# Kernel optimization log

Hardware: AMD Instinct MI355X
Metric: run time of the kernel (lower is better)

## Reference

```python
import jax, jax.numpy as jnp
import numpy as np

B_, L_, D_, N_ = 4, 4096, 64, 16
DT = 0.1
EPS = 1e-6


def _complex_log(x):
    # log|x| (clamped) + i*pi for negative entries, matching torch impl
    real = jnp.log(jnp.maximum(jnp.abs(x), EPS))
    imag = jnp.where(x < 0, jnp.float32(np.pi), jnp.float32(0.0))
    return jax.lax.complex(real, imag)


def _clogaddexp(a, b):
    # stable complex log(exp(a)+exp(b)) using max of real parts
    m = jnp.maximum(a.real, b.real)
    return jnp.log(jnp.exp(a - m) + jnp.exp(b - m)) + m


def _clogcumsumexp(x, axis):
    return jax.lax.associative_scan(_clogaddexp, x, axis=axis)


def setup_inputs() -> dict:
    key = jax.random.key(0)
    ks = jax.random.split(key, 6)
    x = jax.random.normal(ks[0], (B_, L_, D_), jnp.float32)
    s = 1.0 / np.sqrt(D_)
    Wb = jax.random.uniform(ks[1], (N_, D_), jnp.float32, -s, s)
    bb = jax.random.uniform(ks[2], (N_,), jnp.float32, -s, s)
    Wc = jax.random.uniform(ks[3], (N_, D_), jnp.float32, -s, s)
    bc = jax.random.uniform(ks[4], (N_,), jnp.float32, -s, s)
    Wd = jax.random.uniform(ks[5], (1, D_), jnp.float32, -s, s)
    bd = jnp.zeros((1,), jnp.float32)
    # S4D-Real init: A_n = -(n+1), repeated over input_dim rows -> (D, N)
    A = jnp.tile(-(jnp.arange(N_, dtype=jnp.float32) + 1.0)[None, :], (D_, 1))
    return {"x": x, "A": A, "Wb": Wb, "bb": bb, "Wc": Wc, "bc": bc,
            "Wd": Wd, "bd": bd}


def reference(x, A, Wb, bb, Wc, bc, Wd, bd):
    # projections: (b,l,n)
    Bm = x @ Wb.T + bb
    Cm = x @ Wc.T + bc
    # delta network: softplus(linear(x)) + dt, broadcast to input_dim
    delta = jax.nn.softplus(x @ Wd.T + bd) + DT            # (b,l,1)
    dt = jnp.broadcast_to(delta, x.shape)                  # (b,l,d)
    # discretize
    tmp = A * dt[..., None]                                # (b,l,d,n)
    A_bar = jnp.exp(tmp)
    delta_B = jnp.einsum('bld,bln->bldn', dt, Bm)
    B_bar = (A_bar - 1.0) * delta_B / (tmp + EPS)
    term2 = B_bar * x[..., None]                           # (b,l,d,n)
    # parallel scan via complex log-cumsum-exp trick
    log_a = _complex_log(A_bar)
    log_b = _complex_log(term2)
    a_star = jnp.cumsum(log_a, axis=1)                     # (b,l,d,n) complex
    t = _clogcumsumexp(log_b - a_star, axis=1)
    scan = jnp.exp(a_star + t).real                        # (b,l,d,n)
    return jnp.sum(scan * Cm[:, :, None, :], axis=-1)      # (b,l,d)
```

## Files before the change

### kernel.cpp

```cpp
#include <hip/hip_runtime.h>

#define B_ 4
#define L_ 4096
#define D_ 64
#define N_ 16
#define CHUNK 16
#define NCHUNK (L_ / CHUNK)
#define TOTCHUNK (B_ * NCHUNK)

constexpr float DT_  = 0.1f;
constexpr float EPS_ = 1e-6f;

__global__ __launch_bounds__(64) void proj_scan_kernel(
    const float* __restrict__ x,  const float* __restrict__ A,
    const float* __restrict__ Wb, const float* __restrict__ bb,
    const float* __restrict__ Wc, const float* __restrict__ bc,
    const float* __restrict__ Wd, const float* __restrict__ bd,
    float* __restrict__ S, float* __restrict__ Cdec,
    float* __restrict__ Wcor, float* __restrict__ out)
{
    const int gc    = blockIdx.x;
    const int batch = gc >> 8;
    const int c     = gc & (NCHUNK - 1);
    const int lane  = threadIdx.x;
    const int base0 = batch * L_ + c * CHUNK;

    __shared__ float xs[CHUNK * D_];
    __shared__ float ag[CHUNK * 32];
    __shared__ float cm[CHUNK * N_];
    __shared__ float wbuf[CHUNK * N_];

    const float4* xg  = (const float4*)(x + (size_t)base0 * D_);
    float4*       xsv = (float4*)xs;
    #pragma unroll
    for (int i = 0; i < 4; i++) xsv[i * 64 + lane] = xg[i * 64 + lane];

    const int o  = lane & 31;
    const int h2 = lane >> 5;
    float wreg[32];
    const float* Wrow = (o < 16) ? (Wb + o * D_) : (Wc + (o - 16) * D_);
    const float4* w4p = (const float4*)(Wrow + h2 * 32);
    #pragma unroll
    for (int j = 0; j < 8; j++) {
        float4 w4 = w4p[j];
        wreg[4*j+0] = w4.x; wreg[4*j+1] = w4.y;
        wreg[4*j+2] = w4.z; wreg[4*j+3] = w4.w;
    }
    const float wd   = Wd[lane];
    const float bd0  = bd[0];
    const float An   = A[lane & 15];
    const float bias = (o < 16) ? bb[o] : bc[o - 16];

    __syncthreads();

    float r[CHUNK];
    #pragma unroll
    for (int p = 0; p < CHUNK; p++) r[p] = xs[p * D_ + lane] * wd;
    #pragma unroll
    for (int m = 32; m >= 1; m >>= 1) {
        #pragma unroll
        for (int p = 0; p < CHUNK; p++) r[p] += __shfl_xor(r[p], m, 64);
    }
    float delta[CHUNK];
    #pragma unroll
    for (int p = 0; p < CHUNK; p++) {
        float z = r[p] + bd0;
        delta[p] = fmaxf(z, 0.0f) + log1pf(expf(-fabsf(z))) + DT_;
    }

    #pragma unroll
    for (int p = 0; p < CHUNK; p++) {
        float acc = 0.0f;
        const float4* xs4 = (const float4*)(xs + p * D_ + h2 * 32);
        #pragma unroll
        for (int j = 0; j < 8; j++) {
            float4 v = xs4[j];
            acc += v.x * wreg[4*j+0] + v.y * wreg[4*j+1]
                 + v.z * wreg[4*j+2] + v.w * wreg[4*j+3];
        }
        acc += __shfl_xor(acc, 32, 64);
        if (lane < 16) {
            float Bm  = acc + bias;
            float tmp = An * delta[p];
            float a   = expf(tmp);
            float g   = (a - 1.0f) * delta[p] * Bm / (tmp + EPS_);
            ag[p * 32 + lane]      = a;
            ag[p * 32 + 16 + lane] = g;
        } else if (lane < 32) {
            cm[p * 16 + (lane - 16)] = acc + bias;
        }
    }
    __syncthreads();

    float h[N_];
    #pragma unroll
    for (int n = 0; n < N_; n++) h[n] = 0.0f;
    for (int s = 0; s < CHUNK; s++) {
        float xd = xs[s * D_ + lane];
        const float4* row = (const float4*)(ag + s * 32);
        const float4* crw = (const float4*)(cm + s * 16);
        float acc = 0.0f;
        #pragma unroll
        for (int q = 0; q < 4; q++) {
            float4 a4 = row[q];
            float4 g4 = row[4 + q];
            float4 c4 = crw[q];
            h[4*q+0] = a4.x * h[4*q+0] + g4.x * xd;  acc += c4.x * h[4*q+0];
            h[4*q+1] = a4.y * h[4*q+1] + g4.y * xd;  acc += c4.y * h[4*q+1];
            h[4*q+2] = a4.z * h[4*q+2] + g4.z * xd;  acc += c4.z * h[4*q+2];
            h[4*q+3] = a4.w * h[4*q+3] + g4.w * xd;  acc += c4.w * h[4*q+3];
        }
        out[(size_t)(base0 + s) * D_ + lane] = acc;
    }
    #pragma unroll
    for (int n = 0; n < N_; n++)
        S[(size_t)(gc * N_ + n) * D_ + lane] = h[n];

    if (lane < 16) {
        float cumn = 1.0f;
        for (int s = 0; s < CHUNK; s++) {
            cumn *= ag[s * 32 + lane];
            wbuf[s * 16 + lane] = cm[s * 16 + lane] * cumn;
        }
        Cdec[gc * N_ + lane] = cumn;
    }
    __syncthreads();
    ((float4*)(Wcor + (size_t)base0 * 16))[lane] = ((const float4*)wbuf)[lane];
}

#define G_ 32
__global__ __launch_bounds__(64) void combine(
    float* __restrict__ S, const float* __restrict__ Cdec)
{
    const int b = blockIdx.x >> 4;
    const int n = blockIdx.x & 15;
    const int d = threadIdx.x;
    const int cb = b * NCHUNK;

    float*       baseS = S    + (size_t)(cb * N_ + n) * D_ + d;
    const float* baseA = Cdec + cb * N_ + n;

    float run = 0.0f;
    float sbuf[G_], abuf[G_];
    #pragma unroll
    for (int j = 0; j < G_; j++) {
        sbuf[j] = baseS[(size_t)j * (N_ * D_)];
        abuf[j] = baseA[j * N_];
    }
    for (int cc = 0; cc < NCHUNK; cc += G_) {
        const int cn = (cc + G_ < NCHUNK) ? (cc + G_) : cc;
        float t[G_], u[G_];
        #pragma unroll
        for (int j = 0; j < G_; j++) {
            t[j] = baseS[(size_t)(cn + j) * (N_ * D_)];
            u[j] = baseA[(cn + j) * N_];
        }
        #pragma unroll
        for (int j = 0; j < G_; j++) {
            baseS[(size_t)(cc + j) * (N_ * D_)] = run;
            run = abuf[j] * run + sbuf[j];
        }
        #pragma unroll
        for (int j = 0; j < G_; j++) { sbuf[j] = t[j]; abuf[j] = u[j]; }
    }
}

__global__ __launch_bounds__(64) void apply_kernel(
    const float* __restrict__ Wcor, const float* __restrict__ S,
    float* __restrict__ out)
{
    const int gc    = blockIdx.x;
    const int batch = gc >> 8;
    const int c     = gc & (NCHUNK - 1);
    const int lane  = threadIdx.x;
    const int base0 = batch * L_ + c * CHUNK;

    __shared__ float wl[CHUNK * N_];

    ((float4*)wl)[lane] = ((const float4*)(Wcor + (size_t)base0 * 16))[lane];

    float hi[N_];
    #pragma unroll
    for (int n = 0; n < N_; n++)
        hi[n] = S[(size_t)(gc * N_ + n) * D_ + lane];

    float4 ov[4];
    const float4* og = (const float4*)(out + (size_t)base0 * D_);
    #pragma unroll
    for (int i = 0; i < 4; i++) ov[i] = og[i * 64 + lane];

    __syncthreads();

    float acc[CHUNK];
    #pragma unroll
    for (int s = 0; s < CHUNK; s++) {
        const float4* crw = (const float4*)(wl + s * 16);
        float a = 0.0f;
        #pragma unroll
        for (int q = 0; q < 4; q++) {
            float4 w4 = crw[q];
            a += w4.x * hi[4*q+0] + w4.y * hi[4*q+1]
               + w4.z * hi[4*q+2] + w4.w * hi[4*q+3];
        }
        acc[s] = a;
    }

    #pragma unroll
    for (int s = 0; s < CHUNK; s++)
        out[(size_t)(base0 + s) * D_ + lane] = out[(size_t)(base0 + s) * D_ + lane] + acc[s];
}

extern "C" void kernel_launch(void* const* d_in, const int* in_sizes, int n_in,
                              void* d_out, int out_size, void* d_ws, size_t ws_size,
                              hipStream_t stream)
{
    const float* x  = (const float*)d_in[0];
    const float* A  = (const float*)d_in[1];
    const float* Wb = (const float*)d_in[2];
    const float* bb = (const float*)d_in[3];
    const float* Wc = (const float*)d_in[4];
    const float* bc = (const float*)d_in[5];
    const float* Wd = (const float*)d_in[6];
    const float* bd = (const float*)d_in[7];
    float* out = (float*)d_out;

    float* S    = (float*)d_ws;
    float* Cdec = S    + (size_t)TOTCHUNK * N_ * D_;
    float* Wcor = Cdec + (size_t)TOTCHUNK * N_;

    proj_scan_kernel<<<TOTCHUNK, 64, 0, stream>>>(x, A, Wb, bb, Wc, bc, Wd, bd,
                                                  S, Cdec, Wcor, out);
    combine<<<B_ * N_, 64, 0, stream>>>(S, Cdec);
    apply_kernel<<<TOTCHUNK, 64, 0, stream>>>(Wcor, S, out);
}
```

Measured before the change: 103.4 us.

## Split projection and intra-chunk scan into separate kernels with lane-parallel B/C projection

```diff
diff --git a/kernel.cpp b/kernel.cpp
--- a/kernel.cpp
+++ b/kernel.cpp
@@ -7,17 +7,17 @@
 #define CHUNK 16
 #define NCHUNK (L_ / CHUNK)
 #define TOTCHUNK (B_ * NCHUNK)
+#define PROW 48
 
 constexpr float DT_  = 0.1f;
 constexpr float EPS_ = 1e-6f;
 
-__global__ __launch_bounds__(64) void proj_scan_kernel(
+__global__ __launch_bounds__(64) void proj_kernel(
     const float* __restrict__ x,  const float* __restrict__ A,
     const float* __restrict__ Wb, const float* __restrict__ bb,
     const float* __restrict__ Wc, const float* __restrict__ bc,
     const float* __restrict__ Wd, const float* __restrict__ bd,
-    float* __restrict__ S, float* __restrict__ Cdec,
-    float* __restrict__ Wcor, float* __restrict__ out)
+    float* __restrict__ P, float* __restrict__ Wcor, float* __restrict__ Cdec)
 {
     const int gc    = blockIdx.x;
     const int batch = gc >> 8;
@@ -26,8 +26,7 @@
     const int base0 = batch * L_ + c * CHUNK;
 
     __shared__ float xs[CHUNK * D_];
-    __shared__ float ag[CHUNK * 32];
-    __shared__ float cm[CHUNK * N_];
+    __shared__ float pbuf[CHUNK * PROW];
     __shared__ float wbuf[CHUNK * N_];
 
     const float4* xg  = (const float4*)(x + (size_t)base0 * D_);
@@ -35,21 +34,24 @@
     #pragma unroll
     for (int i = 0; i < 4; i++) xsv[i * 64 + lane] = xg[i * 64 + lane];
 
-    const int o  = lane & 31;
-    const int h2 = lane >> 5;
-    float wreg[32];
-    const float* Wrow = (o < 16) ? (Wb + o * D_) : (Wc + (o - 16) * D_);
-    const float4* w4p = (const float4*)(Wrow + h2 * 32);
-    #pragma unroll
-    for (int j = 0; j < 8; j++) {
-        float4 w4 = w4p[j];
-        wreg[4*j+0] = w4.x; wreg[4*j+1] = w4.y;
-        wreg[4*j+2] = w4.z; wreg[4*j+3] = w4.w;
-    }
-    const float wd   = Wd[lane];
-    const float bd0  = bd[0];
-    const float An   = A[lane & 15];
-    const float bias = (o < 16) ? bb[o] : bc[o - 16];
+    const int n  = lane & 15;
+    const int qt = lane >> 4;
+    float wB[16], wC[16];
+    {
+        const float4* wb4 = (const float4*)(Wb + n * D_ + qt * 16);
+        const float4* wc4 = (const float4*)(Wc + n * D_ + qt * 16);
+        #pragma unroll
+        for (int j = 0; j < 4; j++) {
+            float4 b4 = wb4[j], c4 = wc4[j];
+            wB[4*j+0] = b4.x; wB[4*j+1] = b4.y; wB[4*j+2] = b4.z; wB[4*j+3] = b4.w;
+            wC[4*j+0] = c4.x; wC[4*j+1] = c4.y; wC[4*j+2] = c4.z; wC[4*j+3] = c4.w;
+        }
+    }
+    const float wd  = Wd[lane];
+    const float bd0 = bd[0];
+    const float An  = A[n];
+    const float bB  = bb[n];
+    const float bC  = bc[n];
 
     __syncthreads();
 
@@ -68,106 +70,53 @@
         delta[p] = fmaxf(z, 0.0f) + log1pf(expf(-fabsf(z))) + DT_;
     }
 
-    #pragma unroll
-    for (int p = 0; p < CHUNK; p++) {
-        float acc = 0.0f;
-        const float4* xs4 = (const float4*)(xs + p * D_ + h2 * 32);
-        #pragma unroll
-        for (int j = 0; j < 8; j++) {
+    float av[CHUNK], cv[CHUNK];
+    #pragma unroll
+    for (int p = 0; p < CHUNK; p++) {
+        const float4* xs4 = (const float4*)(xs + p * D_ + qt * 16);
+        float accB = 0.0f, accC = 0.0f;
+        #pragma unroll
+        for (int j = 0; j < 4; j++) {
             float4 v = xs4[j];
-            acc += v.x * wreg[4*j+0] + v.y * wreg[4*j+1]
-                 + v.z * wreg[4*j+2] + v.w * wreg[4*j+3];
-        }
-        acc += __shfl_xor(acc, 32, 64);
-        if (lane < 16) {
-            float Bm  = acc + bias;
-            float tmp = An * delta[p];
-            float a   = expf(tmp);
-            float g   = (a - 1.0f) * delta[p] * Bm / (tmp + EPS_);
-            ag[p * 32 + lane]      = a;
-            ag[p * 32 + 16 + lane] = g;
-        } else if (lane < 32) {
-            cm[p * 16 + (lane - 16)] = acc + bias;
-        }
-    }
+            accB += v.x * wB[4*j+0] + v.y * wB[4*j+1] + v.z * wB[4*j+2] + v.w * wB[4*j+3];
+            accC += v.x * wC[4*j+0] + v.y * wC[4*j+1] + v.z * wC[4*j+2] + v.w * wC[4*j+3];
+        }
+        accB += __shfl_xor(accB, 16, 64);  accB += __shfl_xor(accB, 32, 64);
+        accC += __shfl_xor(accC, 16, 64);  accC += __shfl_xor(accC, 32, 64);
+
+        float Bm  = accB + bB;
+        float Cmv = accC + bC;
+        float tmp = An * delta[p];
+        float a   = expf(tmp);
+        float g   = (a - 1.0f) * delta[p] * Bm / (tmp + EPS_);
+        av[p] = a;  cv[p] = Cmv;
+        if      (qt == 0) pbuf[p * PROW + n]      = a;
+        else if (qt == 1) pbuf[p * PROW + 16 + n] = g;
+        else if (qt == 2) pbuf[p * PROW + 32 + n] = Cmv;
+    }
+
+    float cum = 1.0f;
+    #pragma unroll
+    for (int p = 0; p < CHUNK; p++) {
+        cum *= av[p];
+        if (qt == 3) wbuf[p * N_ + n] = cv[p] * cum;
+    }
+    if (qt == 3) Cdec[gc * N_ + n] = cum;
     __syncthreads();
 
-    float h[N_];
-    #pragma unroll
-    for (int n = 0; n < N_; n++) h[n] = 0.0f;
-    for (int s = 0; s < CHUNK; s++) {
-        float xd = xs[s * D_ + lane];
-        const float4* row = (const float4*)(ag + s * 32);
-        const float4* crw = (const float4*)(cm + s * 16);
-        float acc = 0.0f;
-        #pragma unroll
-        for (int q = 0; q < 4; q++) {
-            float4 a4 = row[q];
-            float4 g4 = row[4 + q];
-            float4 c4 = crw[q];
-            h[4*q+0] = a4.x * h[4*q+0] + g4.x * xd;  acc += c4.x * h[4*q+0];
-            h[4*q+1] = a4.y * h[4*q+1] + g4.y * xd;  acc += c4.y * h[4*q+1];
-            h[4*q+2] = a4.z * h[4*q+2] + g4.z * xd;  acc += c4.z * h[4*q+2];
-            h[4*q+3] = a4.w * h[4*q+3] + g4.w * xd;  acc += c4.w * h[4*q+3];
-        }
-        out[(size_t)(base0 + s) * D_ + lane] = acc;
-    }
-    #pragma unroll
-    for (int n = 0; n < N_; n++)
-        S[(size_t)(gc * N_ + n) * D_ + lane] = h[n];
-
-    if (lane < 16) {
-        float cumn = 1.0f;
-        for (int s = 0; s < CHUNK; s++) {
-            cumn *= ag[s * 32 + lane];
-            wbuf[s * 16 + lane] = cm[s * 16 + lane] * cumn;
-        }
-        Cdec[gc * N_ + lane] = cumn;
-    }
-    __syncthreads();
-    ((float4*)(Wcor + (size_t)base0 * 16))[lane] = ((const float4*)wbuf)[lane];
-}
-
-#define G_ 32
-__global__ __launch_bounds__(64) void combine(
-    float* __restrict__ S, const float* __restrict__ Cdec)
-{
-    const int b = blockIdx.x >> 4;
-    const int n = blockIdx.x & 15;
-    const int d = threadIdx.x;
-    const int cb = b * NCHUNK;
-
-    float*       baseS = S    + (size_t)(cb * N_ + n) * D_ + d;
-    const float* baseA = Cdec + cb * N_ + n;
-
-    float run = 0.0f;
-    float sbuf[G_], abuf[G_];
-    #pragma unroll
-    for (int j = 0; j < G_; j++) {
-        sbuf[j] = baseS[(size_t)j * (N_ * D_)];
-        abuf[j] = baseA[j * N_];
-    }
-    for (int cc = 0; cc < NCHUNK; cc += G_) {
-        const int cn = (cc + G_ < NCHUNK) ? (cc + G_) : cc;
-        float t[G_], u[G_];
-        #pragma unroll
-        for (int j = 0; j < G_; j++) {
-            t[j] = baseS[(size_t)(cn + j) * (N_ * D_)];
-            u[j] = baseA[(cn + j) * N_];
-        }
-        #pragma unroll
-        for (int j = 0; j < G_; j++) {
-            baseS[(size_t)(cc + j) * (N_ * D_)] = run;
-            run = abuf[j] * run + sbuf[j];
-        }
-        #pragma unroll
-        for (int j = 0; j < G_; j++) { sbuf[j] = t[j]; abuf[j] = u[j]; }
-    }
-}
-
-__global__ __launch_bounds__(64) void apply_kernel(
-    const float* __restrict__ Wcor, const float* __restrict__ S,
-    float* __restrict__ out)
+    {
+        float4*       Pg  = (float4*)(P + (size_t)gc * (CHUNK * PROW));
+        const float4* pb4 = (const float4*)pbuf;
+        Pg[lane]       = pb4[lane];
+        Pg[64 + lane]  = pb4[64 + lane];
+        Pg[128 + lane] = pb4[128 + lane];
+        ((float4*)(Wcor + (size_t)gc * (CHUNK * N_)))[lane] = ((const float4*)wbuf)[lane];
+    }
+}
+
+__global__ __launch_bounds__(64) void scan_kernel(
+    const float* __restrict__ x, const float* __restrict__ P,
+    float* __restrict__ S, float* __restrict__ out)
 {
     const int gc    = blockIdx.x;
     const int batch = gc >> 8;
@@ -175,39 +124,104 @@
     const int lane  = threadIdx.x;
     const int base0 = batch * L_ + c * CHUNK;
 
-    __shared__ float wl[CHUNK * N_];
-
-    ((float4*)wl)[lane] = ((const float4*)(Wcor + (size_t)base0 * 16))[lane];
+    float xq[CHUNK];
+    #pragma unroll
+    for (int p = 0; p < CHUNK; p++)
+        xq[p] = x[(size_t)(base0 + p) * D_ + lane];
+
+    const float* pp = P + (size_t)gc * (CHUNK * PROW);
+
+    float h[N_];
+    #pragma unroll
+    for (int i = 0; i < N_; i++) h[i] = 0.0f;
+
+    #pragma unroll
+    for (int p = 0; p < CHUNK; p++) {
+        const float4* row = (const float4*)(pp + p * PROW);
+        float acc = 0.0f;
+        #pragma unroll
+        for (int q = 0; q < 4; q++) {
+            float4 a4 = row[q];
+            float4 g4 = row[4 + q];
+            float4 c4 = row[8 + q];
+            h[4*q+0] = a4.x * h[4*q+0] + g4.x * xq[p];  acc += c4.x * h[4*q+0];
+            h[4*q+1] = a4.y * h[4*q+1] + g4.y * xq[p];  acc += c4.y * h[4*q+1];
+            h[4*q+2] = a4.z * h[4*q+2] + g4.z * xq[p];  acc += c4.z * h[4*q+2];
+            h[4*q+3] = a4.w * h[4*q+3] + g4.w * xq[p];  acc += c4.w * h[4*q+3];
+        }
+        out[(size_t)(base0 + p) * D_ + lane] = acc;
+    }
+    #pragma unroll
+    for (int i = 0; i < N_; i++)
+        S[(size_t)(gc * N_ + i) * D_ + lane] = h[i];
+}
+
+#define G_ 32
+__global__ __launch_bounds__(64) void combine(
+    float* __restrict__ S, const float* __restrict__ Cdec)
+{
+    const int b = blockIdx.x >> 4;
+    const int n = blockIdx.x & 15;
+    const int d = threadIdx.x;
+    const int cb = b * NCHUNK;
+
+    float*       baseS = S    + (size_t)(cb * N_ + n) * D_ + d;
+    const float* baseA = Cdec + cb * N_ + n;
+
+    float run = 0.0f;
+    float sbuf[G_], abuf[G_];
+    #pragma unroll
+    for (int j = 0; j < G_; j++) {
+        sbuf[j] = baseS[(size_t)j * (N_ * D_)];
+        abuf[j] = baseA[j * N_];
+    }
+    for (int cc = 0; cc < NCHUNK; cc += G_) {
+        const int cn = (cc + G_ < NCHUNK) ? (cc + G_) : cc;
+        float t[G_], u[G_];
+        #pragma unroll
+        for (int j = 0; j < G_; j++) {
+            t[j] = baseS[(size_t)(cn + j) * (N_ * D_)];
+            u[j] = baseA[(cn + j) * N_];
+        }
+        #pragma unroll
+        for (int j = 0; j < G_; j++) {
+            baseS[(size_t)(cc + j) * (N_ * D_)] = run;
+            run = abuf[j] * run + sbuf[j];
+        }
+        #pragma unroll
+        for (int j = 0; j < G_; j++) { sbuf[j] = t[j]; abuf[j] = u[j]; }
+    }
+}
+
+__global__ __launch_bounds__(64) void apply_kernel(
+    const float* __restrict__ Wcor, const float* __restrict__ S,
+    float* __restrict__ out)
+{
+    const int gc    = blockIdx.x;
+    const int batch = gc >> 8;
+    const int c     = gc & (NCHUNK - 1);
+    const int lane  = threadIdx.x;
+    const int base0 = batch * L_ + c * CHUNK;
 
     float hi[N_];
     #pragma unroll
-    for (int n = 0; n < N_; n++)
-        hi[n] = S[(size_t)(gc * N_ + n) * D_ + lane];
-
-    float4 ov[4];
-    const float4* og = (const float4*)(out + (size_t)base0 * D_);
-    #pragma unroll
-    for (int i = 0; i < 4; i++) ov[i] = og[i * 64 + lane];
-
-    __syncthreads();
-
-    float acc[CHUNK];
-    #pragma unroll
-    for (int s = 0; s < CHUNK; s++) {
-        const float4* crw = (const float4*)(wl + s * 16);
-        float a = 0.0f;
+    for (int i = 0; i < N_; i++)
+        hi[i] = S[(size_t)(gc * N_ + i) * D_ + lane];
+
+    const float* wrow = Wcor + (size_t)gc * (CHUNK * N_);
+    #pragma unroll
+    for (int p = 0; p < CHUNK; p++) {
+        const float4* w4 = (const float4*)(wrow + p * N_);
+        float acc = 0.0f;
         #pragma unroll
         for (int q = 0; q < 4; q++) {
-            float4 w4 = crw[q];
-            a += w4.x * hi[4*q+0] + w4.y * hi[4*q+1]
-               + w4.z * hi[4*q+2] + w4.w * hi[4*q+3];
-        }
-        acc[s] = a;
-    }
-
-    #pragma unroll
-    for (int s = 0; s < CHUNK; s++)
-        out[(size_t)(base0 + s) * D_ + lane] = out[(size_t)(base0 + s) * D_ + lane] + acc[s];
+            float4 w = w4[q];
+            acc += w.x * hi[4*q+0] + w.y * hi[4*q+1]
+                 + w.z * hi[4*q+2] + w.w * hi[4*q+3];
+        }
+        const size_t idx = (size_t)(base0 + p) * D_ + lane;
+        out[idx] = out[idx] + acc;
+    }
 }
 
 extern "C" void kernel_launch(void* const* d_in, const int* in_sizes, int n_in,
@@ -224,12 +238,14 @@
     const float* bd = (const float*)d_in[7];
     float* out = (float*)d_out;
 
-    float* S    = (float*)d_ws;
+    float* P    = (float*)d_ws;
+    float* Wcor = P    + (size_t)TOTCHUNK * CHUNK * PROW;
+    float* S    = Wcor + (size_t)TOTCHUNK * CHUNK * N_;
     float* Cdec = S    + (size_t)TOTCHUNK * N_ * D_;
-    float* Wcor = Cdec + (size_t)TOTCHUNK * N_;
-
-    proj_scan_kernel<<<TOTCHUNK, 64, 0, stream>>>(x, A, Wb, bb, Wc, bc, Wd, bd,
-                                                  S, Cdec, Wcor, out);
+
+    proj_kernel<<<TOTCHUNK, 64, 0, stream>>>(x, A, Wb, bb, Wc, bc, Wd, bd,
+                                             P, Wcor, Cdec);
+    scan_kernel<<<TOTCHUNK, 64, 0, stream>>>(x, P, S, out);
     combine<<<B_ * N_, 64, 0, stream>>>(S, Cdec);
     apply_kernel<<<TOTCHUNK, 64, 0, stream>>>(Wcor, S, out);
 }
```

Result: slower. 117.2 us (+13.4%).
